# Kernel optimization log

Hardware: AMD Instinct MI355X
Metric: run time of the kernel (lower is better)

Reference implementation:

```python
import jax, jax.numpy as jnp
import numpy as np

N_HEAD = 16
T0 = 1.0        # eta schedule reference time
C_LOG = 3.0     # fixed eta(t) = C_LOG * log(t / T0)  (mode='log', non-learnable default)
ETA_CLIP = 50.0 # eta clamped to [-ETA_CLIP, ETA_CLIP] before exponentiation


def setup_inputs() -> dict:
    key = jax.random.key(0)
    k0, k1, k2 = jax.random.split(key, 3)
    B, T, D = 2, 2048, 1024
    x = jax.random.normal(k0, (B, T, D), dtype=jnp.float32)
    ln_weight = jnp.ones((D,), dtype=jnp.float32)  # LayerNorm weight (bias=False per cfg)
    c_attn_w = jax.random.normal(k1, (3 * D, D), dtype=jnp.float32) * 0.02  # torch Linear weight [3D, D]
    c_proj_w = jax.random.normal(k2, (D, D), dtype=jnp.float32) * 0.02      # output proj [D, D]
    # theta_h = inv_softplus(1.0) so that step size h = softplus(theta_h) = 1.0
    theta_h = jnp.asarray(np.log(np.expm1(1.0)), dtype=jnp.float32)
    return {"x": x, "ln_weight": ln_weight, "c_attn_w": c_attn_w,
            "c_proj_w": c_proj_w, "theta_h": theta_h}


def _layer_norm(x, w, eps=1e-5):
    mu = jnp.mean(x, axis=-1, keepdims=True)
    var = jnp.var(x, axis=-1, keepdims=True)
    return (x - mu) * jax.lax.rsqrt(var + eps) * w


def reference(x, ln_weight, c_attn_w, c_proj_w, theta_h):
    B, T, D = x.shape
    H = N_HEAD
    hd = D // H

    y = _layer_norm(x, ln_weight)
    qkv = jnp.einsum('btd,ed->bte', y, c_attn_w)        # [B, T, 3D]
    q, k, v = jnp.split(qkv, 3, axis=-1)
    q = q.reshape(B, T, H, hd).transpose(0, 2, 1, 3)    # [B, H, T, hd]
    k = k.reshape(B, T, H, hd).transpose(0, 2, 1, 3)
    v = v.reshape(B, T, H, hd).transpose(0, 2, 1, 3)

    # time-dependent conformal/symplectic scaling: t_i = t0 + h*i, eta = c_log*log(t/t0)
    h = jax.nn.softplus(theta_h)
    t = T0 + h * jnp.arange(T, dtype=jnp.float32)
    eta = jnp.clip(C_LOG * jnp.log(t / T0), -ETA_CLIP, ETA_CLIP)  # [T]
    q = q * jnp.exp(eta)[None, None, :, None]    # query scaled by exp(+eta(t_i))
    k = k * jnp.exp(-eta)[None, None, :, None]   # key scaled by exp(-eta(t_j))

    att = jnp.einsum('bhqd,bhkd->bhqk', q, k) / jnp.sqrt(jnp.float32(hd))
    mask = jnp.tril(jnp.ones((T, T), dtype=bool))  # causal: keep j <= i
    att = jnp.where(mask[None, None], att, -jnp.inf)
    att = jax.nn.softmax(att, axis=-1)

    out = jnp.einsum('bhqk,bhkd->bhqd', att, v)
    out = out.transpose(0, 2, 1, 3).reshape(B, T, D)
    return jnp.einsum('btd,ed->bte', out, c_proj_w)
```

## Files before the change

kernel.cpp:

```cpp
#include <hip/hip_runtime.h>
#include <stdint.h>
#include <stddef.h>

typedef __attribute__((ext_vector_type(8))) short short8;
typedef __attribute__((ext_vector_type(4))) float float4v;

#define T_SEQ 2048
#define D_MODEL 1024
#define NH 16
#define HD 64

static __device__ __forceinline__ unsigned short f2bf(float f) {
  unsigned u = __builtin_bit_cast(unsigned, f);
  u += 0x7fffu + ((u >> 16) & 1u);
  return (unsigned short)(u >> 16);
}
static __device__ __forceinline__ float bf2f(unsigned short h) {
  unsigned u = ((unsigned)h) << 16;
  return __builtin_bit_cast(float, u);
}
static __device__ __forceinline__ float4v mfma16(short8 a, short8 b, float4v c) {
  return __builtin_amdgcn_mfma_f32_16x16x32_bf16(a, b, c, 0, 0, 0);
}
static __device__ __forceinline__ void split3(float f, unsigned short& h0,
                                              unsigned short& h1, unsigned short& h2) {
  h0 = f2bf(f);
  float r1 = f - bf2f(h0);
  h1 = f2bf(r1);
  float r2 = r1 - bf2f(h1);
  h2 = f2bf(r2);
}
static __device__ __forceinline__ void split2(float f, unsigned short& h0, unsigned short& h1) {
  h0 = f2bf(f);
  h1 = f2bf(f - bf2f(h0));
}

static __device__ __forceinline__ void stage16(const unsigned short* g, unsigned short* l) {
#if __has_builtin(__builtin_amdgcn_global_load_lds)
  __builtin_amdgcn_global_load_lds(
      (const __attribute__((address_space(1))) unsigned int*)g,
      (__attribute__((address_space(3))) unsigned int*)l, 16, 0, 0);
#else
  *(short8*)l = *(const short8*)g;
#endif
}

__global__ __launch_bounds__(256) void prep_kernel(
    const float* x, const float* wgt, const float* attn_w, const float* theta,
    unsigned short* y0, unsigned short* y1, unsigned short* y2,
    unsigned short* W0, unsigned short* W1, unsigned short* W2,
    float* E, float* Einv) {
  __shared__ float rs[4], rq[4];
  int bx = blockIdx.x;
  int tid = threadIdx.x;
  if (bx < 4096) {
    int row = bx;
    const float* xr = x + (size_t)row * D_MODEL;
    float v[4];
    float sum = 0.f, ssq = 0.f;
    for (int it = 0; it < 4; ++it) {
      float f = xr[tid + 256 * it];
      v[it] = f;
      sum += f; ssq += f * f;
    }
    for (int off = 32; off >= 1; off >>= 1) {
      sum += __shfl_xor(sum, off, 64);
      ssq += __shfl_xor(ssq, off, 64);
    }
    int w = tid >> 6;
    if ((tid & 63) == 0) { rs[w] = sum; rq[w] = ssq; }
    __syncthreads();
    sum = rs[0] + rs[1] + rs[2] + rs[3];
    ssq = rq[0] + rq[1] + rq[2] + rq[3];
    float mu = sum * (1.0f / D_MODEL);
    float var = ssq * (1.0f / D_MODEL) - mu * mu;
    float rstd = rsqrtf(var + 1e-5f);
    for (int it = 0; it < 4; ++it) {
      int d = tid + 256 * it;
      float y = (v[it] - mu) * rstd * wgt[d];
      unsigned short h0, h1, h2;
      split3(y, h0, h1, h2);
      size_t o = (size_t)row * D_MODEL + d;
      y0[o] = h0; y1[o] = h1; y2[o] = h2;
    }
  } else if (bx < 5632) {
    size_t base = ((size_t)(bx - 4096) * 256 + tid) * 8;
    int row = (int)(base >> 10);
    short8 a, b, c;
    for (int j = 0; j < 8; ++j) {
      unsigned short h0, h1, h2;
      split3(attn_w[base + j], h0, h1, h2);
      a[j] = (short)h0; b[j] = (short)h1; c[j] = (short)h2;
    }
    *(short8*)(W0 + base) = a;
    *(short8*)(W1 + base) = b;
    if (row < 2048) *(short8*)(W2 + base) = c;
  } else {
    int i = (bx - 5632) * 256 + tid;
    if (i < T_SEQ) {
      float th = theta[0];
      float h = log1pf(expf(th));
      float t = 1.0f + h * (float)i;
      float eta = 3.0f * logf(t);
      eta = fminf(fmaxf(eta, -50.0f), 50.0f);
      E[i] = expf(eta);
      Einv[i] = expf(-eta);
    }
  }
}

__global__ __launch_bounds__(256) void conv_pw(const float* src, unsigned short* P0,
                                               unsigned short* P1) {
  size_t base = ((size_t)blockIdx.x * 256 + threadIdx.x) * 8;
  short8 a, b;
  for (int j = 0; j < 8; ++j) {
    unsigned short h0, h1;
    split2(src[base + j], h0, h1);
    a[j] = (short)h0; b[j] = (short)h1;
  }
  *(short8*)(P0 + base) = a;
  *(short8*)(P1 + base) = b;
}


template <int MA, int MB, int KS>
static __device__ __forceinline__ void mfma_row2(float4v (&acc)[4][4],
                                                 const short8 (&afr)[4][2],
                                                 const short8 (&bfr)[4][2]) {
  __builtin_amdgcn_s_setprio(1);
#pragma unroll
  for (int nf = 0; nf < 4; ++nf)
    acc[MA][nf] = mfma16(afr[MA][KS], bfr[nf][KS], acc[MA][nf]);
#pragma unroll
  for (int nf = 0; nf < 4; ++nf)
    acc[MB][nf] = mfma16(afr[MB][KS], bfr[nf][KS], acc[MB][nf]);
  __builtin_amdgcn_s_setprio(0);
}

#define RD_A(BF, MF, KS)                                                        \
  (*(const short8*)(lds_u + (BF) * 24576 + ((wm * 64 + (MF) * 16 + ln) * 64) +  \
                    ((((KS) * 4 + q4) ^ lnl) * 8)))
#define RD_B(BF, NF, KS)                                                        \
  (*(const short8*)(lds_u + (BF) * 24576 + 16384 +                              \
                    ((wn * 64 + (NF) * 16 + ln) * 64) +                         \
                    ((((KS) * 4 + q4) ^ lnl) * 8)))

#define STG_A(BF, AP, KI)                                                       \
  do {                                                                          \
    const unsigned short* g0 = (AP) + (size_t)(m0 + srow8) * 1024 + (KI) + scol8; \
    stage16(g0, lds_u + (BF) * 24576 + tid * 8);                                \
    stage16(g0 + 64 * 1024, lds_u + (BF) * 24576 + 4096 + tid * 8);             \
    stage16(g0 + 128 * 1024, lds_u + (BF) * 24576 + 8192 + tid * 8);            \
    stage16(g0 + 192 * 1024, lds_u + (BF) * 24576 + 12288 + tid * 8);           \
  } while (0)

#define STG_B(BF, BP, KI)                                                       \
  do {                                                                          \
    const unsigned short* g0 = (BP) + (size_t)(brow0 + srow8) * 1024 + (KI) + scol8; \
    stage16(g0, lds_u + (BF) * 24576 + 16384 + tid * 8);                        \
    stage16(g0 + 64 * 1024, lds_u + (BF) * 24576 + 16384 + 4096 + tid * 8);     \
  } while (0)

#define ASEL(tb) ((tb) == 5 ? y2 : (((tb) & 1) ? y1 : y0))
#define BSEL(tb) (isV ? ((tb) < 2 ? W0 : W1)                                    \
                      : ((tb) < 2 ? W0 : ((tb) < 4 ? W1 : ((tb) == 4 ? W2 : W0))))

#define SBAR __builtin_amdgcn_s_barrier()
#define SCHED0 __builtin_amdgcn_sched_barrier(0)

#define PHASES4(BF, A2P, B2P, KI2)                                              \
                       \
  afr[0][0] = RD_A(BF, 0, 0); afr[1][0] = RD_A(BF, 1, 0);                       \
  bfr[0][0] = RD_B(BF, 0, 0); bfr[1][0] = RD_B(BF, 1, 0);                       \
  bfr[2][0] = RD_B(BF, 2, 0); bfr[3][0] = RD_B(BF, 3, 0);                       \
  SCHED0; SBAR;                                                                 \
  mfma_row2<0, 1, 0>(acc, afr, bfr);                                            \
  SCHED0; SBAR;                                                                 \
                       \
  afr[2][0] = RD_A(BF, 2, 0); afr[3][0] = RD_A(BF, 3, 0);                       \
  afr[0][1] = RD_A(BF, 0, 1); afr[1][1] = RD_A(BF, 1, 1);                       \
  afr[2][1] = RD_A(BF, 2, 1); afr[3][1] = RD_A(BF, 3, 1);                       \
  SCHED0; SBAR;                                                                 \
  mfma_row2<2, 3, 0>(acc, afr, bfr);                                            \
  SCHED0; SBAR;                                                                 \
          \
  bfr[0][1] = RD_B(BF, 0, 1); bfr[1][1] = RD_B(BF, 1, 1);                       \
  bfr[2][1] = RD_B(BF, 2, 1); bfr[3][1] = RD_B(BF, 3, 1);                       \
  if (pref) { STG_A(BF, A2P, KI2); }                                            \
  SCHED0; SBAR;                                                                 \
  mfma_row2<0, 1, 1>(acc, afr, bfr);                                            \
  SCHED0; SBAR;                                                                 \
             \
  if (pref) { STG_B(BF, B2P, KI2); }                                            \
  SCHED0; SBAR;                                                                 \
  mfma_row2<2, 3, 1>(acc, afr, bfr);                                            \
  SCHED0;                                                                       \
  if (pref) { asm volatile("s_waitcnt vmcnt(6)" ::: "memory"); }                \
  else      { asm volatile("s_waitcnt vmcnt(0)" ::: "memory"); }                \
  SBAR;

__global__ __launch_bounds__(512, 2) void qkv8(
    const unsigned short* __restrict__ y0, const unsigned short* __restrict__ y1,
    const unsigned short* __restrict__ y2, const unsigned short* __restrict__ W0,
    const unsigned short* __restrict__ W1, const unsigned short* __restrict__ W2,
    const float* __restrict__ E, const float* __restrict__ Einv,
    float* __restrict__ Qf, unsigned short* __restrict__ K0,
    unsigned short* __restrict__ K1, unsigned short* __restrict__ K2,
    unsigned short* __restrict__ VbT) {
  extern __shared__ unsigned short lds_u[];
  int tid = threadIdx.x;
  int w = tid >> 6, lane = tid & 63, q4 = lane >> 4, ln = lane & 15;
  int lnl = ln & 7;
  int wm = w >> 1, wn = w & 1;

  int bid = blockIdx.x, bx, by;
  if (bid < 256) {
    int wg = ((bid & 7) << 5) | (bid >> 3);
    by = wg >> 4; bx = wg & 15;
  } else {
    int vid = bid - 256;
    int wg = ((vid & 7) << 4) | (vid >> 3);
    by = wg >> 3; bx = 16 + (wg & 7);
  }
  int m0 = by * 256;
  bool isV = (bx >= 16);
  int NKT = isV ? 48 : 96;
  int brow0 = isV ? (2048 + (bx - 16) * 128) : bx * 128;

  int srow8 = tid >> 3;
  int scol8 = ((tid & 7) ^ (srow8 & 7)) * 8;

  float4v zero = {0.f, 0.f, 0.f, 0.f};
  float4v acc[4][4];
#pragma unroll
  for (int mf = 0; mf < 4; ++mf)
#pragma unroll
    for (int nf = 0; nf < 4; ++nf) acc[mf][nf] = zero;
  short8 afr[4][2], bfr[4][2];

  {
    const unsigned short* Ap = ASEL(0);
    const unsigned short* Bp = BSEL(0);
    STG_A(0, Ap, 0);
    STG_B(0, Bp, 0);
    STG_A(1, Ap, 64);
    STG_B(1, Bp, 64);
  }
  asm volatile("s_waitcnt vmcnt(6)" ::: "memory");
  SBAR;

  int NIT = NKT >> 1;
  for (int it = 0; it < NIT; ++it) {
    const int a2 = 2 * it + 2;
    const bool pref = (a2 < NKT);
    const unsigned short *Aa2 = y0, *Ba2 = W0, *Ab2 = y0, *Bb2 = W0;
    int kia2 = 0, kib2 = 0;
    if (pref) {
      int ta = a2 >> 4, tb = (a2 + 1) >> 4;
      Aa2 = ASEL(ta); Ba2 = BSEL(ta); kia2 = (a2 & 15) << 6;
      Ab2 = ASEL(tb); Bb2 = BSEL(tb); kib2 = ((a2 + 1) & 15) << 6;
    }
    PHASES4(0, Aa2, Ba2, kia2)
    PHASES4(1, Ab2, Bb2, kib2)
  }

  int bi = m0 >> 11, m0g = m0 & 2047;
  if (bx < 8) {
    float* Ql = (float*)lds_u;
    for (int g = 0; g < 2; ++g) {
      if (wn == g) {
#pragma unroll
        for (int mf = 0; mf < 4; ++mf)
#pragma unroll
          for (int nf = 0; nf < 4; ++nf)
#pragma unroll
            for (int r = 0; r < 4; ++r) {
              int rl = wm * 64 + mf * 16 + q4 * 4 + r;
              int t = m0g + rl;
              Ql[rl * 64 + nf * 16 + ln] = acc[mf][nf][r] * (E[t] * 0.1803368801f);
            }
      }
      __syncthreads();
      int h = bx * 2 + g;
      float* dst = Qf + ((size_t)(bi * NH + h) * T_SEQ + m0g) * HD;
      for (int itc = 0; itc < 8; ++itc) {
        int idx = itc * 512 + tid;
        *(float4v*)(dst + idx * 4) = *(const float4v*)(Ql + idx * 4);
      }
      __syncthreads();
    }
  } else if (bx < 16) {
    unsigned short* Kl = lds_u;
    for (int g = 0; g < 2; ++g) {
      if (wn == g) {
#pragma unroll
        for (int mf = 0; mf < 4; ++mf)
#pragma unroll
          for (int nf = 0; nf < 4; ++nf)
#pragma unroll
            for (int r = 0; r < 4; ++r) {
              int rl = wm * 64 + mf * 16 + q4 * 4 + r;
              int t = m0g + rl;
              unsigned short h0, h1, h2;
              split3(acc[mf][nf][r] * Einv[t], h0, h1, h2);
              int o = rl * 64 + nf * 16 + ln;
              Kl[o] = h0; Kl[16384 + o] = h1; Kl[32768 + o] = h2;
            }
      }
      __syncthreads();
      int h = (bx - 8) * 2 + g;
      size_t base = ((size_t)(bi * NH + h) * T_SEQ + m0g) * HD;
      for (int itc = 0; itc < 4; ++itc) {
        int idx = itc * 512 + tid;
        *(short8*)(K0 + base + idx * 8) = *(const short8*)(Kl + idx * 8);
        *(short8*)(K1 + base + idx * 8) = *(const short8*)(Kl + 16384 + idx * 8);
        *(short8*)(K2 + base + idx * 8) = *(const short8*)(Kl + 32768 + idx * 8);
      }
      __syncthreads();
    }
  } else {
    unsigned short* Vl = lds_u;
    for (int g = 0; g < 2; ++g) {
      if (wn == g) {
#pragma unroll
        for (int mf = 0; mf < 4; ++mf)
#pragma unroll
          for (int nf = 0; nf < 4; ++nf)
#pragma unroll
            for (int r = 0; r < 4; ++r) {
              int rl = wm * 64 + mf * 16 + q4 * 4 + r;
              int d = nf * 16 + ln;
              Vl[d * 256 + rl] = f2bf(acc[mf][nf][r]);
            }
      }
      __syncthreads();
      int h = (bx - 16) * 2 + g;
      unsigned short* dst = VbT + (size_t)(bi * NH + h) * HD * T_SEQ + m0g;
      for (int itc = 0; itc < 4; ++itc) {
        int idx = itc * 512 + tid;
        int d = idx >> 5, c = idx & 31;
        *(short8*)(dst + (size_t)d * T_SEQ + c * 8) = *(const short8*)(Vl + d * 256 + c * 8);
      }
      __syncthreads();
    }
  }
}
#undef RD_A
#undef RD_B
#undef STG_A
#undef STG_B
#undef ASEL
#undef BSEL
#undef PHASES4
#undef SBAR
#undef SCHED0

#define ATTN_STAGE(BUF, J0)                                                   \
  for (int i_ = 0; i_ < 2; ++i_) {                                            \
    size_t go_ = (size_t)((J0) + srow + i_ * 32) * 64 + scd * 8;              \
    int lo_ = tid * 8 + i_ * 2048;                                            \
    stage16(Kb0 + go_, &Ks[BUF][0][lo_]);                                     \
    stage16(Kb1 + go_, &Ks[BUF][1][lo_]);                                     \
    stage16(Kb2 + go_, &Ks[BUF][2][lo_]);                                     \
    stage16(Vb + (size_t)(srow + i_ * 32) * T_SEQ + (J0) + scd * 8,           \
            &Vs[BUF][lo_]);                                                   \
  }

#define ATTN_STEP(JT, DIAG)                                                   \
  {                                                                           \
    const int cur_ = (JT) & 1;                                                \
    float p[4][4];                                                            \
    for (int c = 0; c < 4; ++c) {                                             \
      float4v s = zero;                                                       \
      for (int ks = 0; ks < 2; ++ks) {                                        \
        int koff = ((c * 16 + ln) * 8 + ((ks * 4 + q4) ^ swz)) * 8;           \
        short8 k0v = *(const short8*)&Ks[cur_][0][koff];                      \
        short8 k1v = *(const short8*)&Ks[cur_][1][koff];                      \
        short8 k2v = *(const short8*)&Ks[cur_][2][koff];                      \
        s = mfma16(qa[ks][0], k0v, s);                                        \
        s = mfma16(qa[ks][1], k0v, s);                                        \
        s = mfma16(qa[ks][0], k1v, s);                                        \
        s = mfma16(qa[ks][1], k1v, s);                                        \
        s = mfma16(qa[ks][0], k2v, s);                                        \
        s = mfma16(qa[ks][2], k0v, s);                                        \
      }                                                                       \
      if (DIAG) {                                                             \
        int jrow = (JT) * 64 + c * 16 + ln;                                   \
        for (int r = 0; r < 4; ++r)                                           \
          if (jrow > ibase + q4 * 4 + r) s[r] = -3e38f;                       \
      }                                                                       \
      for (int r = 0; r < 4; ++r) p[c][r] = s[r];                             \
    }                                                                         \
    float alpha[4], mnew[4];                                                  \
    for (int r = 0; r < 4; ++r) {                                             \
      float tm = fmaxf(fmaxf(p[0][r], p[1][r]), fmaxf(p[2][r], p[3][r]));     \
      for (int off = 8; off >= 1; off >>= 1)                                  \
        tm = fmaxf(tm, __shfl_xor(tm, off, 16));                              \
      mnew[r] = fmaxf(m_r[r], tm);                                            \
      alpha[r] = exp2f(m_r[r] - mnew[r]);                                     \
      m_r[r] = mnew[r];                                                       \
    }                                                                         \
    for (int c = 0; c < 4; ++c)                                               \
      for (int r = 0; r < 4; ++r) p[c][r] = exp2f(p[c][r] - mnew[r]);         \
    for (int c = 0; c < 4; ++c)                                               \
      for (int r = 0; r < 4; ++r) oacc[c][r] *= alpha[r];                     \
    for (int r = 0; r < 4; ++r) lacc[r] *= alpha[r];                          \
    __asm__ __volatile__("" ::: "memory");                                    \
    for (int c = 0; c < 4; ++c)                                               \
      for (int r = 0; r < 4; ++r)                                             \
        Plds[w][q4 * 4 + r][c * 16 + ln] =                                    \
            (unsigned short)(__builtin_bit_cast(unsigned, p[c][r]) >> 16);    \
    __asm__ __volatile__("" ::: "memory");                                    \
    for (int ks = 0; ks < 2; ++ks) {                                          \
      short8 pa = *(const short8*)&Plds[w][ln][ks * 32 + q4 * 8];             \
      for (int c = 0; c < 4; ++c) {                                           \
        int voff = ((c * 16 + ln) * 8 + ((ks * 4 + q4) ^ swz)) * 8;           \
        short8 vb = *(const short8*)&Vs[cur_][voff];                          \
        oacc[c] = mfma16(pa, vb, oacc[c]);                                    \
      }                                                                       \
      lacc = mfma16(pa, ones, lacc);                                          \
    }                                                                         \
    __asm__ __volatile__("" ::: "memory");                                    \
  }

__global__ __launch_bounds__(256) void attn_kernel(
    const float* Qf, const unsigned short* K0, const unsigned short* K1,
    const unsigned short* K2, const unsigned short* VbT,
    unsigned short* Ob0, unsigned short* Ob1) {
  __shared__ unsigned short Ks[2][3][4096];
  __shared__ unsigned short Vs[2][4096];
  __shared__ unsigned short Plds[4][16][72];
  int tid = threadIdx.x;
  int w = tid >> 6, lane = tid & 63, q4 = lane >> 4, ln = lane & 15;
  int bidx = blockIdx.x;
  int bh = ((bidx & 7) << 2) | ((bidx >> 3) & 3);
  int px = bidx >> 5;
  const float* Qb = Qf + (size_t)bh * T_SEQ * HD;
  const unsigned short* Kb0 = K0 + (size_t)bh * T_SEQ * HD;
  const unsigned short* Kb1 = K1 + (size_t)bh * T_SEQ * HD;
  const unsigned short* Kb2 = K2 + (size_t)bh * T_SEQ * HD;
  const unsigned short* Vb = VbT + (size_t)bh * HD * T_SEQ;
  int b = bh >> 4, hh = bh & 15;
  float4v zero = {0.f, 0.f, 0.f, 0.f};
  short8 ones;
  for (int j = 0; j < 8; ++j) ones[j] = (short)(unsigned short)0x3F80;

  int srow = tid >> 3, scs = tid & 7;
  int scd = scs ^ (srow & 7);
  int swz = ln & 7;

  for (int half = 0; half < 2; ++half) {
    int qt = half ? (31 - px) : px;
    int q0 = qt * 64;
    int ibase = q0 + w * 16;

    short8 qa[2][3];
    {
      const float* qp = Qb + (size_t)(ibase + ln) * HD;
      for (int ks = 0; ks < 2; ++ks) {
        float f[8];
        *(float4v*)&f[0] = *(const float4v*)(qp + ks * 32 + q4 * 8);
        *(float4v*)&f[4] = *(const float4v*)(qp + ks * 32 + q4 * 8 + 4);
        for (int j = 0; j < 8; ++j) {
          unsigned short h0, h1, h2;
          split3(f[j], h0, h1, h2);
          qa[ks][0][j] = (short)h0; qa[ks][1][j] = (short)h1; qa[ks][2][j] = (short)h2;
        }
      }
    }

    float m_r[4] = {-3e38f, -3e38f, -3e38f, -3e38f};
    float4v lacc = zero;
    float4v oacc[4];
    for (int c = 0; c < 4; ++c) oacc[c] = zero;

    __syncthreads();
    ATTN_STAGE(0, 0)
    for (int jt = 0; jt < qt; ++jt) {
      __syncthreads();
      ATTN_STAGE((jt + 1) & 1, (jt + 1) * 64)
      ATTN_STEP(jt, 0)
    }
    __syncthreads();
    ATTN_STEP(qt, 1)

    for (int c = 0; c < 4; ++c)
      for (int r = 0; r < 4; ++r) {
        int i = ibase + q4 * 4 + r;
        float val = oacc[c][r] / lacc[r];
        unsigned short h0, h1;
        split2(val, h0, h1);
        size_t o = ((size_t)(b * T_SEQ + i)) * D_MODEL + hh * 64 + c * 16 + ln;
        Ob0[o] = h0; Ob1[o] = h1;
      }
  }
}
#undef ATTN_STAGE
#undef ATTN_STEP

__global__ __launch_bounds__(256) void proj_gemm(
    const unsigned short* A0, const unsigned short* A1,
    const unsigned short* P0, const unsigned short* P1, float* out) {
  __shared__ unsigned short SB[4 * 4096];
  int tid = threadIdx.x;
  int w = tid >> 6, lane = tid & 63, q4 = lane >> 4, ln = lane & 15;
  int wr = w >> 1, wc = w & 1;
  int n0g = blockIdx.x * 128;
  int m0 = blockIdx.y * 128;
  const unsigned short* Asrc[2] = {A0, A1};
  const unsigned short* Bsrc[2] = {P0, P1};

  float4v zero = {0.f, 0.f, 0.f, 0.f};
  float4v acc[4][4];
  for (int mt = 0; mt < 4; ++mt)
    for (int ct = 0; ct < 4; ++ct) acc[mt][ct] = zero;

  int srow = tid >> 2, kpart = tid & 3;
  unsigned lds_off = (unsigned)tid * 16;

  for (int k0 = 0; k0 < D_MODEL; k0 += 32) {
    __syncthreads();
    for (int i = 0; i < 2; ++i) {
      size_t arow = (size_t)(m0 + srow + i * 64) * D_MODEL + k0 + kpart * 8;
      size_t brow = (size_t)(n0g + srow + i * 64) * D_MODEL + k0 + kpart * 8;
      for (int s = 0; s < 2; ++s) {
        stage16(Asrc[s] + arow, (unsigned short*)((char*)(SB + s * 4096) + lds_off + i * 4096));
        stage16(Bsrc[s] + brow, (unsigned short*)((char*)(SB + (2 + s) * 4096) + lds_off + i * 4096));
      }
    }
    __syncthreads();

    short8 af[4][2];
    for (int mt = 0; mt < 4; ++mt)
      for (int s = 0; s < 2; ++s)
        af[mt][s] = *(const short8*)(SB + s * 4096 + (wr * 64 + mt * 16 + ln) * 32 + q4 * 8);
    for (int ct = 0; ct < 4; ++ct) {
      int brow = (wc * 64 + ct * 16 + ln) * 32 + q4 * 8;
      short8 b0 = *(const short8*)(SB + 2 * 4096 + brow);
      short8 b1 = *(const short8*)(SB + 3 * 4096 + brow);
      for (int mt = 0; mt < 4; ++mt) {
        float4v a = acc[mt][ct];
        a = mfma16(af[mt][0], b0, a);
        a = mfma16(af[mt][1], b0, a);
        a = mfma16(af[mt][0], b1, a);
        acc[mt][ct] = a;
      }
    }
  }

  for (int mt = 0; mt < 4; ++mt)
    for (int ct = 0; ct < 4; ++ct)
      for (int r = 0; r < 4; ++r) {
        int gm = m0 + wr * 64 + mt * 16 + q4 * 4 + r;
        int col = n0g + wc * 64 + ct * 16 + ln;
        out[(size_t)gm * D_MODEL + col] = acc[mt][ct][r];
      }
}

extern "C" void kernel_launch(void* const* d_in, const int* in_sizes, int n_in,
                              void* d_out, int out_size, void* d_ws, size_t ws_size,
                              hipStream_t stream) {
  const float* x      = (const float*)d_in[0];
  const float* ln_w   = (const float*)d_in[1];
  const float* attn_w = (const float*)d_in[2];
  const float* proj_w = (const float*)d_in[3];
  const float* theta  = (const float*)d_in[4];
  float* out = (float*)d_out;

  char* ws = (char*)d_ws;
  const size_t SZY  = (size_t)4096 * 1024 * 2;
  const size_t SZW  = (size_t)3072 * 1024 * 2;
  const size_t SZW2 = (size_t)2048 * 1024 * 2;
  const size_t SZQ  = (size_t)2 * 16 * 2048 * 64 * 4;
  const size_t SZK  = (size_t)2 * 16 * 2048 * 64 * 2;

  unsigned short* y0 = (unsigned short*)(ws);
  unsigned short* y1 = (unsigned short*)(ws + SZY);
  unsigned short* y2 = (unsigned short*)(ws + 2 * SZY);
  unsigned short* W0 = (unsigned short*)(ws + 3 * SZY);
  unsigned short* W1 = (unsigned short*)(ws + 3 * SZY + SZW);
  unsigned short* W2 = (unsigned short*)(ws + 3 * SZY + 2 * SZW);
  float* Qf          = (float*)(ws + 3 * SZY + 2 * SZW + SZW2);
  unsigned short* K0 = (unsigned short*)(ws + 3 * SZY + 2 * SZW + SZW2 + SZQ);
  unsigned short* K1 = (unsigned short*)(ws + 3 * SZY + 2 * SZW + SZW2 + SZQ + SZK);
  float* E           = (float*)(ws + 3 * SZY + 2 * SZW + SZW2 + SZQ + 2 * SZK);
  float* Einv        = E + T_SEQ;
  unsigned short* Ob0 = y0;
  unsigned short* Ob1 = y1;
  unsigned short* PW0 = y2;
  unsigned short* PW1 = y2 + (size_t)1024 * 1024;
  unsigned short* VbT = (unsigned short*)d_out;
  unsigned short* K2  = (unsigned short*)((char*)d_out + SZK);

  size_t needed = 3 * SZY + 2 * SZW + SZW2 + SZQ + 2 * SZK + 2 * T_SEQ * 4;
  if (ws_size < needed) return;

  static int lds_cfg = 0;
  if (!lds_cfg) {
    hipFuncSetAttribute((const void*)qkv8,
                        hipFuncAttributeMaxDynamicSharedMemorySize, 98304);
    lds_cfg = 1;
  }

  prep_kernel<<<dim3(5640), dim3(256), 0, stream>>>(x, ln_w, attn_w, theta,
                                                    y0, y1, y2, W0, W1, W2, E, Einv);
  qkv8<<<dim3(384), dim3(512), 98304, stream>>>(y0, y1, y2, W0, W1, W2, E, Einv,
                                                Qf, K0, K1, K2, VbT);
  conv_pw<<<dim3(512), dim3(256), 0, stream>>>(proj_w, PW0, PW1);
  attn_kernel<<<dim3(512), dim3(256), 0, stream>>>(Qf, K0, K1, K2, VbT, Ob0, Ob1);
  proj_gemm<<<dim3(8, 32), dim3(256), 0, stream>>>(Ob0, Ob1, PW0, PW1, out);
}
```

Measured before the change: 384.8 us.

## Restructure QKV GEMM main loop to 4-slot K32 pipeline with depth-3 prefetch

The QKV projection GEMM's K-loop moves from a 2-buffer, K=64-per-stage scheme with four interleaved read/MFMA sub-phases to a 4-slot ring of K=32 stages. Each phase loads all fragments, issues the prefetch three stages ahead, then runs 16 MFMAs back to back. The aim is deeper global-load latency hiding and simpler LDS read scheduling. In exchange there are twice as many barriers per K, and ds_reads no longer overlap MFMAs within a stage because of the explicit lgkmcnt(0) wait.

```diff
diff --git a/kernel.cpp b/kernel.cpp
--- a/kernel.cpp
+++ b/kernel.cpp
@@ -123,42 +123,26 @@
 }
 
 
-template <int MA, int MB, int KS>
-static __device__ __forceinline__ void mfma_row2(float4v (&acc)[4][4],
-                                                 const short8 (&afr)[4][2],
-                                                 const short8 (&bfr)[4][2]) {
-  __builtin_amdgcn_s_setprio(1);
-#pragma unroll
-  for (int nf = 0; nf < 4; ++nf)
-    acc[MA][nf] = mfma16(afr[MA][KS], bfr[nf][KS], acc[MA][nf]);
-#pragma unroll
-  for (int nf = 0; nf < 4; ++nf)
-    acc[MB][nf] = mfma16(afr[MB][KS], bfr[nf][KS], acc[MB][nf]);
-  __builtin_amdgcn_s_setprio(0);
-}
-
-#define RD_A(BF, MF, KS)                                                        \
-  (*(const short8*)(lds_u + (BF) * 24576 + ((wm * 64 + (MF) * 16 + ln) * 64) +  \
-                    ((((KS) * 4 + q4) ^ lnl) * 8)))
-#define RD_B(BF, NF, KS)                                                        \
-  (*(const short8*)(lds_u + (BF) * 24576 + 16384 +                              \
-                    ((wn * 64 + (NF) * 16 + ln) * 64) +                         \
-                    ((((KS) * 4 + q4) ^ lnl) * 8)))
-
-#define STG_A(BF, AP, KI)                                                       \
+#define RD_A(SL, MF)                                                            \
+  (*(const short8*)(lds_u + (SL) * 12288 + ((wm * 64 + (MF) * 16 + ln) * 32) +  \
+                    ((q4 ^ (ln & 3)) * 8)))
+#define RD_B(SL, NF)                                                            \
+  (*(const short8*)(lds_u + (SL) * 12288 + 8192 +                               \
+                    ((wn * 64 + (NF) * 16 + ln) * 32) + ((q4 ^ (ln & 3)) * 8)))
+
+#define STG_A(SL, AP, KI)                                                       \
   do {                                                                          \
-    const unsigned short* g0 = (AP) + (size_t)(m0 + srow8) * 1024 + (KI) + scol8; \
-    stage16(g0, lds_u + (BF) * 24576 + tid * 8);                                \
-    stage16(g0 + 64 * 1024, lds_u + (BF) * 24576 + 4096 + tid * 8);             \
-    stage16(g0 + 128 * 1024, lds_u + (BF) * 24576 + 8192 + tid * 8);            \
-    stage16(g0 + 192 * 1024, lds_u + (BF) * 24576 + 12288 + tid * 8);           \
+    const unsigned short* g0 =                                                  \
+        (AP) + (size_t)(m0 + srow4) * 1024 + (KI) + scol4;                      \
+    stage16(g0, lds_u + (SL) * 12288 + tid * 8);                                \
+    stage16(g0 + 128 * 1024, lds_u + (SL) * 12288 + 4096 + tid * 8);            \
   } while (0)
 
-#define STG_B(BF, BP, KI)                                                       \
+#define STG_B(SL, BP, KI)                                                       \
   do {                                                                          \
-    const unsigned short* g0 = (BP) + (size_t)(brow0 + srow8) * 1024 + (KI) + scol8; \
-    stage16(g0, lds_u + (BF) * 24576 + 16384 + tid * 8);                        \
-    stage16(g0 + 64 * 1024, lds_u + (BF) * 24576 + 16384 + 4096 + tid * 8);     \
+    const unsigned short* g0 =                                                  \
+        (BP) + (size_t)(brow0 + srow4) * 1024 + (KI) + scol4;                   \
+    stage16(g0, lds_u + (SL) * 12288 + 8192 + tid * 8);                         \
   } while (0)
 
 #define ASEL(tb) ((tb) == 5 ? y2 : (((tb) & 1) ? y1 : y0))
@@ -168,36 +152,47 @@
 #define SBAR __builtin_amdgcn_s_barrier()
 #define SCHED0 __builtin_amdgcn_sched_barrier(0)
 
-#define PHASES4(BF, A2P, B2P, KI2)                                              \
-                       \
-  afr[0][0] = RD_A(BF, 0, 0); afr[1][0] = RD_A(BF, 1, 0);                       \
-  bfr[0][0] = RD_B(BF, 0, 0); bfr[1][0] = RD_B(BF, 1, 0);                       \
-  bfr[2][0] = RD_B(BF, 2, 0); bfr[3][0] = RD_B(BF, 3, 0);                       \
-  SCHED0; SBAR;                                                                 \
-  mfma_row2<0, 1, 0>(acc, afr, bfr);                                            \
-  SCHED0; SBAR;                                                                 \
-                       \
-  afr[2][0] = RD_A(BF, 2, 0); afr[3][0] = RD_A(BF, 3, 0);                       \
-  afr[0][1] = RD_A(BF, 0, 1); afr[1][1] = RD_A(BF, 1, 1);                       \
-  afr[2][1] = RD_A(BF, 2, 1); afr[3][1] = RD_A(BF, 3, 1);                       \
-  SCHED0; SBAR;                                                                 \
-  mfma_row2<2, 3, 0>(acc, afr, bfr);                                            \
-  SCHED0; SBAR;                                                                 \
-          \
-  bfr[0][1] = RD_B(BF, 0, 1); bfr[1][1] = RD_B(BF, 1, 1);                       \
-  bfr[2][1] = RD_B(BF, 2, 1); bfr[3][1] = RD_B(BF, 3, 1);                       \
-  if (pref) { STG_A(BF, A2P, KI2); }                                            \
-  SCHED0; SBAR;                                                                 \
-  mfma_row2<0, 1, 1>(acc, afr, bfr);                                            \
-  SCHED0; SBAR;                                                                 \
-             \
-  if (pref) { STG_B(BF, B2P, KI2); }                                            \
-  SCHED0; SBAR;                                                                 \
-  mfma_row2<2, 3, 1>(acc, afr, bfr);                                            \
-  SCHED0;                                                                       \
-  if (pref) { asm volatile("s_waitcnt vmcnt(6)" ::: "memory"); }                \
-  else      { asm volatile("s_waitcnt vmcnt(0)" ::: "memory"); }                \
-  SBAR;
+#define PHASE(SLOT)                                                             \
+  {                                                                             \
+    short8 a0 = RD_A(SLOT, 0), a1 = RD_A(SLOT, 1);                              \
+    short8 a2 = RD_A(SLOT, 2), a3 = RD_A(SLOT, 3);                              \
+    short8 b0 = RD_B(SLOT, 0), b1 = RD_B(SLOT, 1);                              \
+    short8 b2 = RD_B(SLOT, 2), b3 = RD_B(SLOT, 3);                              \
+    bool pref = (t + 3 < NKT);                                                  \
+    if (pref) {                                                                 \
+      int tt = t + 3, tb = tt >> 5, ki = (tt & 31) << 5;                        \
+      const unsigned short* Ap = ASEL(tb);                                      \
+      const unsigned short* Bp = BSEL(tb);                                      \
+      STG_A((SLOT + 3) & 3, Ap, ki);                                            \
+      STG_B((SLOT + 3) & 3, Bp, ki);                                            \
+    }                                                                           \
+    SCHED0; SBAR;                                                               \
+    asm volatile("s_waitcnt lgkmcnt(0)" ::: "memory");                          \
+    SCHED0;                                                                     \
+    __builtin_amdgcn_s_setprio(1);                                              \
+    acc[0][0] = mfma16(a0, b0, acc[0][0]);                                      \
+    acc[0][1] = mfma16(a0, b1, acc[0][1]);                                      \
+    acc[0][2] = mfma16(a0, b2, acc[0][2]);                                      \
+    acc[0][3] = mfma16(a0, b3, acc[0][3]);                                      \
+    acc[1][0] = mfma16(a1, b0, acc[1][0]);                                      \
+    acc[1][1] = mfma16(a1, b1, acc[1][1]);                                      \
+    acc[1][2] = mfma16(a1, b2, acc[1][2]);                                      \
+    acc[1][3] = mfma16(a1, b3, acc[1][3]);                                      \
+    acc[2][0] = mfma16(a2, b0, acc[2][0]);                                      \
+    acc[2][1] = mfma16(a2, b1, acc[2][1]);                                      \
+    acc[2][2] = mfma16(a2, b2, acc[2][2]);                                      \
+    acc[2][3] = mfma16(a2, b3, acc[2][3]);                                      \
+    acc[3][0] = mfma16(a3, b0, acc[3][0]);                                      \
+    acc[3][1] = mfma16(a3, b1, acc[3][1]);                                      \
+    acc[3][2] = mfma16(a3, b2, acc[3][2]);                                      \
+    acc[3][3] = mfma16(a3, b3, acc[3][3]);                                      \
+    __builtin_amdgcn_s_setprio(0);                                              \
+    SCHED0;                                                                     \
+    if (pref) { asm volatile("s_waitcnt vmcnt(6)" ::: "memory"); }              \
+    else      { asm volatile("s_waitcnt vmcnt(0)" ::: "memory"); }              \
+    SBAR;                                                                       \
+    ++t;                                                                        \
+  }
 
 __global__ __launch_bounds__(512, 2) void qkv8(
     const unsigned short* __restrict__ y0, const unsigned short* __restrict__ y1,
@@ -210,7 +205,6 @@
   extern __shared__ unsigned short lds_u[];
   int tid = threadIdx.x;
   int w = tid >> 6, lane = tid & 63, q4 = lane >> 4, ln = lane & 15;
-  int lnl = ln & 7;
   int wm = w >> 1, wn = w & 1;
 
   int bid = blockIdx.x, bx, by;
@@ -224,11 +218,11 @@
   }
   int m0 = by * 256;
   bool isV = (bx >= 16);
-  int NKT = isV ? 48 : 96;
+  int NKT = isV ? 96 : 192;
   int brow0 = isV ? (2048 + (bx - 16) * 128) : bx * 128;
 
-  int srow8 = tid >> 3;
-  int scol8 = ((tid & 7) ^ (srow8 & 7)) * 8;
+  int srow4 = tid >> 2;
+  int scol4 = ((tid & 3) ^ (srow4 & 3)) * 8;
 
   float4v zero = {0.f, 0.f, 0.f, 0.f};
   float4v acc[4][4];
@@ -236,32 +230,24 @@
   for (int mf = 0; mf < 4; ++mf)
 #pragma unroll
     for (int nf = 0; nf < 4; ++nf) acc[mf][nf] = zero;
-  short8 afr[4][2], bfr[4][2];
 
   {
     const unsigned short* Ap = ASEL(0);
     const unsigned short* Bp = BSEL(0);
-    STG_A(0, Ap, 0);
-    STG_B(0, Bp, 0);
-    STG_A(1, Ap, 64);
-    STG_B(1, Bp, 64);
+    STG_A(0, Ap, 0);  STG_B(0, Ap == Ap ? Bp : Bp, 0);
+    STG_A(1, Ap, 32); STG_B(1, Bp, 32);
+    STG_A(2, Ap, 64); STG_B(2, Bp, 64);
   }
   asm volatile("s_waitcnt vmcnt(6)" ::: "memory");
   SBAR;
 
-  int NIT = NKT >> 1;
-  for (int it = 0; it < NIT; ++it) {
-    const int a2 = 2 * it + 2;
-    const bool pref = (a2 < NKT);
-    const unsigned short *Aa2 = y0, *Ba2 = W0, *Ab2 = y0, *Bb2 = W0;
-    int kia2 = 0, kib2 = 0;
-    if (pref) {
-      int ta = a2 >> 4, tb = (a2 + 1) >> 4;
-      Aa2 = ASEL(ta); Ba2 = BSEL(ta); kia2 = (a2 & 15) << 6;
-      Ab2 = ASEL(tb); Bb2 = BSEL(tb); kib2 = ((a2 + 1) & 15) << 6;
-    }
-    PHASES4(0, Aa2, Ba2, kia2)
-    PHASES4(1, Ab2, Bb2, kib2)
+  int t = 0;
+  int nit = NKT >> 2;
+  for (int it = 0; it < nit; ++it) {
+    PHASE(0)
+    PHASE(1)
+    PHASE(2)
+    PHASE(3)
   }
 
   int bi = m0 >> 11, m0g = m0 & 2047;
@@ -276,8 +262,8 @@
 #pragma unroll
             for (int r = 0; r < 4; ++r) {
               int rl = wm * 64 + mf * 16 + q4 * 4 + r;
-              int t = m0g + rl;
-              Ql[rl * 64 + nf * 16 + ln] = acc[mf][nf][r] * (E[t] * 0.1803368801f);
+              int tg = m0g + rl;
+              Ql[rl * 64 + nf * 16 + ln] = acc[mf][nf][r] * (E[tg] * 0.1803368801f);
             }
       }
       __syncthreads();
@@ -300,9 +286,9 @@
 #pragma unroll
             for (int r = 0; r < 4; ++r) {
               int rl = wm * 64 + mf * 16 + q4 * 4 + r;
-              int t = m0g + rl;
+              int tg = m0g + rl;
               unsigned short h0, h1, h2;
-              split3(acc[mf][nf][r] * Einv[t], h0, h1, h2);
+              split3(acc[mf][nf][r] * Einv[tg], h0, h1, h2);
               int o = rl * 64 + nf * 16 + ln;
               Kl[o] = h0; Kl[16384 + o] = h1; Kl[32768 + o] = h2;
             }
@@ -351,7 +337,7 @@
 #undef STG_B
 #undef ASEL
 #undef BSEL
-#undef PHASES4
+#undef PHASE
 #undef SBAR
 #undef SCHED0
 
```

New measurement: 407.3 us. 1.06x slower.
